# Optimization experiments

Hardware: AMD Instinct MI355X
Metric: run time of the kernel (lower is better)

Reference implementation:

```python
import jax, jax.numpy as jnp
import numpy as np

WEIGHT = 1.0  # configer affinity_loss weight


def setup_inputs() -> dict:
    key = jax.random.key(0)
    k1, k2, k3, k4, k5 = jax.random.split(key, 5)
    bz, C, h, w = 4, 21, 32, 32
    token_n = h * w            # 1024
    total_n = token_n + 1      # 1025 (CLS token in encoder attns)
    head_n = 8
    return {
        "preds": jax.random.normal(k1, (bz, C, h, w), dtype=jnp.float32),
        "low_feats": jnp.zeros((1,), dtype=jnp.float32),
        "high_feats": jnp.zeros((1,), dtype=jnp.float32),
        "unlabeled_ROIs": jax.random.randint(k2, (bz, h, w), 0, 2, dtype=jnp.int32),
        "targets": jax.random.randint(k3, (bz, h, w), 0, C),
        # raw (pre-renormalization) positive attention maps, stacked over 2 layers
        "attns": jax.random.uniform(k4, (2, bz, head_n, total_n, total_n), dtype=jnp.float32),
        "decode_attns": jax.random.uniform(k5, (2, bz, head_n, token_n, token_n), dtype=jnp.float32),
    }


def reference(preds, low_feats, high_feats, unlabeled_ROIs, targets, attns, decode_attns):
    # loss_index=2, gt_add=0
    bz, C, h, w = preds.shape
    token_n = h * w
    Le = attns.shape[0]
    Ld = decode_attns.shape[0]

    # Encoder attentions: drop CLS row/col, row-normalize, average over heads & layers.
    enc = attns[:, :, :, 1:, 1:]                         # (Le, b, H, t, t)
    enc = enc / enc.sum(axis=-1, keepdims=True)
    encode_attn_avg = enc.mean(axis=(0, 2))              # (b, t, t)

    # Decoder attentions: crop to token_n, row-normalize, average over heads & layers.
    dec = decode_attns[:, :, :, :token_n, :token_n]
    dec = dec / dec.sum(axis=-1, keepdims=True)
    decode_attn_avg = dec.mean(axis=(0, 2))              # (b, t, t)

    total_attn_avg = (encode_attn_avg * Le + decode_attn_avg * Ld) / (Le + Ld)

    # Class probabilities per token: (b, t, C)
    prob = jax.nn.softmax(preds, axis=1).reshape(bz, C, token_n).transpose(0, 2, 1)

    # The broadcast-multiply-sum over dim=2 is exactly a batched matmul.
    affinity_prob = jnp.einsum('bij,bjc->bic', total_attn_avg, prob)
    affinity_prob = affinity_prob / affinity_prob.sum(axis=-1, keepdims=True)

    # nearest-interp to (h, w) is the identity here (ROIs already at (h, w))
    roi = unlabeled_ROIs.astype(jnp.float32).reshape(bz, token_n, 1)
    N = roi.sum()
    loss = (roi * jnp.abs(prob - affinity_prob)).sum()
    loss = jnp.where(N > 0, loss / N, loss)
    return WEIGHT * loss
```

## Files before the change

### kernel.cpp

```cpp
#include <hip/hip_runtime.h>
#include <cstdint>
#include <cstddef>

#define C_N     21
#define BZ      4
#define TOKEN_N 1024
#define TOTAL_N 1025
#define PROB_ELEMS (BZ * TOKEN_N * C_N)
#define ENC_TOT  67240000u

typedef short  short8 __attribute__((ext_vector_type(8)));
typedef float  f32x4  __attribute__((ext_vector_type(4)));

static __device__ __forceinline__ unsigned int f2bf(float x) {
    unsigned int u = __float_as_uint(x);
    return (u + 0x7FFFu + ((u >> 16) & 1u)) >> 16;
}

__global__ __launch_bounds__(256) void softmax_kernel(const float* __restrict__ preds,
                                                      float* __restrict__ prob) {
    int t = blockIdx.x * blockDim.x + threadIdx.x;
    if (t >= BZ * TOKEN_N) return;
    int b = t >> 10, j = t & 1023;
    const float* p = preds + (size_t)b * C_N * TOKEN_N + j;
    float v[C_N];
    float mx = -3.4e38f;
#pragma unroll
    for (int c = 0; c < C_N; ++c) { v[c] = p[(size_t)c * TOKEN_N]; mx = fmaxf(mx, v[c]); }
    float ss = 0.f;
#pragma unroll
    for (int c = 0; c < C_N; ++c) { v[c] = __expf(v[c] - mx); ss += v[c]; }
    float inv = 1.f / ss;
    float* o = prob + (size_t)t * C_N;
#pragma unroll
    for (int c = 0; c < C_N; ++c) o[c] = v[c] * inv;
}

__global__ __launch_bounds__(256) void bpack2_kernel(const float* __restrict__ prob,
                                                     uint4* __restrict__ bp) {
    int idx = blockIdx.x * 256 + threadIdx.x;
    if (idx >= BZ * 32 * 2 * 64) return;
    int lane = idx & 63;
    int nt   = (idx >> 6) & 1;
    int kk   = (idx >> 7) & 31;
    int b    = idx >> 12;
    int n    = (lane & 15) + nt * 16;
    int k0   = kk * 32 + ((lane >> 4) << 3);
    unsigned int h[8];
#pragma unroll
    for (int e = 0; e < 8; ++e) {
        float v;
        if (n < C_N)       v = prob[((size_t)b * TOKEN_N + (k0 + e)) * C_N + n];
        else if (n == C_N) v = 1.0f;
        else               v = 0.0f;
        h[e] = f2bf(v);
    }
    uint4 o;
    o.x = h[0] | (h[1] << 16);
    o.y = h[2] | (h[3] << 16);
    o.z = h[4] | (h[5] << 16);
    o.w = h[6] | (h[7] << 16);
    bp[idx] = o;
}

template<bool ENC>
__device__ __forceinline__ void rows_body(const float* __restrict__ base, int mm, int lane,
                                          int i0, const uint4* __restrict__ bp,
                                          float* __restrict__ acc, float* __restrict__ ldsw) {
    constexpr int NSLOT = ENC ? 5 : 4;
    constexpr int D     = ENC ? 3 : 4;
    constexpr int RS    = 68;
    const int b = (mm >> 3) & 3;

    const float* gs[NSLOT];
    int lt[NSLOT];
#pragma unroll
    for (int s = 0; s < NSLOT; ++s) {
        if constexpr (ENC) {
            int t = (s == 4) ? (256 + (lane & 15)) : (s * 64 + lane);
            int row = t / 17, u = t - row * 17;
            size_t start = (size_t)mm * 1050625u + (size_t)(1 + i0 + row) * 1025u + 1u;
            int delta = (int)(start & 3);
            size_t gidx = start - delta + (size_t)u * 4;
            if (s == 4 && gidx > (size_t)(ENC_TOT - 964)) gidx = ENC_TOT - 964;
            gs[s] = base + gidx;
            lt[s] = t * 4;
        } else {
            int t = s * 64 + lane;
            int row = t >> 4, u = t & 15;
            gs[s] = base + (size_t)mm * 1048576u + (size_t)(i0 + row) * 1024u + (size_t)u * 4;
            lt[s] = row * RS + u * 4;
        }
    }

    float4 G[D][NSLOT];
    uint4  Bb[2][4];
    const uint4* bpp = bp + (size_t)b * 4096 + lane;

    const int r = lane & 15, kg = lane >> 4;
    int fragbase;
    if constexpr (ENC) fragbase = r * RS + ((mm + i0 + r + 2) & 3) + kg * 8;
    else               fragbase = r * RS + kg * 8;

    f32x4 c0 = {0.f, 0.f, 0.f, 0.f};
    f32x4 c1 = {0.f, 0.f, 0.f, 0.f};

    auto KSTEP = [&](const float* lf, int j0, uint4 bb0, uint4 bb1) {
        float a0, a1, a2, a3, a4, a5, a6, a7;
        if constexpr (ENC) {
            const float* p = lf + fragbase + j0;
            a0 = p[0]; a1 = p[1]; a2 = p[2]; a3 = p[3];
            a4 = p[4]; a5 = p[5]; a6 = p[6]; a7 = p[7];
        } else {
            float4 lo = *reinterpret_cast<const float4*>(lf + fragbase + j0);
            float4 hi = *reinterpret_cast<const float4*>(lf + fragbase + j0 + 4);
            a0 = lo.x; a1 = lo.y; a2 = lo.z; a3 = lo.w;
            a4 = hi.x; a5 = hi.y; a6 = hi.z; a7 = hi.w;
        }
        uint4 aw;
        aw.x = f2bf(a0) | (f2bf(a1) << 16);
        aw.y = f2bf(a2) | (f2bf(a3) << 16);
        aw.z = f2bf(a4) | (f2bf(a5) << 16);
        aw.w = f2bf(a6) | (f2bf(a7) << 16);
        short8 af = __builtin_bit_cast(short8, aw);
        c0 = __builtin_amdgcn_mfma_f32_16x16x32_bf16(af, __builtin_bit_cast(short8, bb0), c0, 0, 0, 0);
        c1 = __builtin_amdgcn_mfma_f32_16x16x32_bf16(af, __builtin_bit_cast(short8, bb1), c1, 0, 0, 0);
    };

#pragma unroll
    for (int s = 0; s < D; ++s)
#pragma unroll
        for (int q = 0; q < NSLOT; ++q)
            G[s][q] = *reinterpret_cast<const float4*>(gs[q] + s * 64);
#pragma unroll
    for (int q = 0; q < 4; ++q) Bb[0][q] = bpp[q * 64];
    {
        float* d0 = ldsw;
#pragma unroll
        for (int q = 0; q < NSLOT; ++q)
            *reinterpret_cast<float4*>(d0 + lt[q]) = G[0][q];
    }
#pragma unroll
    for (int q = 0; q < 4; ++q) Bb[1][q] = bpp[256 + q * 64];

#pragma unroll
    for (int k = 0; k < 16; ++k) {
        const float* lf = ldsw + (k & 1) * 1088;
        KSTEP(lf, 0,  Bb[k & 1][0], Bb[k & 1][1]);
        KSTEP(lf, 32, Bb[k & 1][2], Bb[k & 1][3]);
        if (k < 15) {
            float* d = ldsw + ((k + 1) & 1) * 1088;
#pragma unroll
            for (int q = 0; q < NSLOT; ++q)
                *reinterpret_cast<float4*>(d + lt[q]) = G[(k + 1) % D][q];
        }
        if (k + D < 16) {
#pragma unroll
            for (int q = 0; q < NSLOT; ++q)
                G[k % D][q] = *reinterpret_cast<const float4*>(gs[q] + (k + D) * 64);
        }
        if (k + 2 < 16) {
#pragma unroll
            for (int q = 0; q < 4; ++q) Bb[k & 1][q] = bpp[(k + 2) * 256 + q * 64];
        }
    }

#pragma unroll
    for (int rr = 0; rr < 4; ++rr) {
        float sv  = __shfl(c1[rr], (lane & 48) + 5);
        float inv = 1.0f / sv;
        int i = i0 + kg * 4 + rr;
        float* ao = acc + ((size_t)b * TOKEN_N + i) * C_N;
        unsafeAtomicAdd(&ao[r], c0[rr] * inv);
        if (r < C_N - 16) unsafeAtomicAdd(&ao[16 + r], c1[rr] * inv);
    }
}

__global__ __launch_bounds__(256) void rows6_kernel(const float* __restrict__ attns,
                                                    const float* __restrict__ dattns,
                                                    const uint4* __restrict__ bp,
                                                    float* __restrict__ acc) {
    __shared__ __align__(16) float lds[8704];
    const int lane = threadIdx.x & 63;
    const int wv   = threadIdx.x >> 6;
    float* ldsw = lds + wv * 2176;
    const int wid  = blockIdx.x * 4 + wv;
    const int m    = wid >> 6;
    const int i0   = (wid & 63) << 4;
    if (m < 64) rows_body<true >(attns,  m,      lane, i0, bp, acc, ldsw);
    else        rows_body<false>(dattns, m - 64, lane, i0, bp, acc, ldsw);
}

__global__ __launch_bounds__(256) void loss_kernel(const float* __restrict__ prob,
                                                   const float* __restrict__ acc,
                                                   const int* __restrict__ roi,
                                                   float* __restrict__ scal) {
    int t = blockIdx.x * 256 + threadIdx.x;
    float lossp = 0.f, np = 0.f;
    if (t < BZ * TOKEN_N) {
        int rv = roi[t];
        np = (float)rv;
        const float* a = acc + (size_t)t * C_N;
        const float* p = prob + (size_t)t * C_N;
        float S = 0.f;
#pragma unroll
        for (int c = 0; c < C_N; ++c) S += a[c];
        float invS = 1.f / S;
        float l = 0.f;
#pragma unroll
        for (int c = 0; c < C_N; ++c) l += fabsf(p[c] - a[c] * invS);
        lossp = rv ? l : 0.f;
    }
#pragma unroll
    for (int off = 32; off > 0; off >>= 1) {
        lossp += __shfl_down(lossp, off);
        np    += __shfl_down(np, off);
    }
    __shared__ float redL[4], redN[4];
    int lane = threadIdx.x & 63, wv = threadIdx.x >> 6;
    if (lane == 0) { redL[wv] = lossp; redN[wv] = np; }
    __syncthreads();
    if (threadIdx.x == 0) {
        float L  = redL[0] + redL[1] + redL[2] + redL[3];
        float NN = redN[0] + redN[1] + redN[2] + redN[3];
        unsafeAtomicAdd(&scal[0], L);
        unsafeAtomicAdd(&scal[1], NN);
    }
}

__global__ void finalize_kernel(const float* __restrict__ scal, float* __restrict__ out) {
    float loss = scal[0], N = scal[1];
    out[0] = (N > 0.f) ? (loss / N) : loss;
}

extern "C" void kernel_launch(void* const* d_in, const int* in_sizes, int n_in,
                              void* d_out, int out_size, void* d_ws, size_t ws_size,
                              hipStream_t stream) {
    const float* preds  = (const float*)d_in[0];
    const int*   roi    = (const int*)d_in[3];
    const float* attns  = (const float*)d_in[5];
    const float* dattns = (const float*)d_in[6];

    float* prob = (float*)d_ws;
    float* acc  = prob + PROB_ELEMS;
    float* scal = acc + PROB_ELEMS;
    uint4* bpack = (uint4*)((char*)d_ws + ((PROB_ELEMS * 2 + 2) * sizeof(float) + 15 & ~(size_t)15));

    hipMemsetAsync(acc, 0, (PROB_ELEMS + 2) * sizeof(float), stream);

    hipLaunchKernelGGL(softmax_kernel, dim3((BZ * TOKEN_N + 255) / 256), dim3(256), 0, stream,
                       preds, prob);
    hipLaunchKernelGGL(bpack2_kernel, dim3(64), dim3(256), 0, stream,
                       prob, bpack);
    hipLaunchKernelGGL(rows6_kernel, dim3(2048), dim3(256), 0, stream,
                       attns, dattns, bpack, acc);
    hipLaunchKernelGGL(loss_kernel, dim3((BZ * TOKEN_N + 255) / 256), dim3(256), 0, stream,
                       prob, acc, roi, scal);
    hipLaunchKernelGGL(finalize_kernel, dim3(1), dim3(1), 0, stream,
                       scal, (float*)d_out);
}
```

Measured before the change: 129.7 us.

## Load attention row tiles directly into LDS and split K across waves

```diff
diff --git a/kernel.cpp b/kernel.cpp
--- a/kernel.cpp
+++ b/kernel.cpp
@@ -7,10 +7,13 @@
 #define TOKEN_N 1024
 #define TOTAL_N 1025
 #define PROB_ELEMS (BZ * TOKEN_N * C_N)
-#define ENC_TOT  67240000u
+#define ENC_TOT  67240000ull
 
 typedef short  short8 __attribute__((ext_vector_type(8)));
 typedef float  f32x4  __attribute__((ext_vector_type(4)));
+
+typedef __attribute__((address_space(1))) const unsigned int* gld_gp;
+typedef __attribute__((address_space(3))) unsigned int*       gld_lp;
 
 static __device__ __forceinline__ unsigned int f2bf(float x) {
     unsigned int u = __float_as_uint(x);
@@ -64,56 +67,70 @@
 }
 
 template<bool ENC>
-__device__ __forceinline__ void rows_body(const float* __restrict__ base, int mm, int lane,
-                                          int i0, const uint4* __restrict__ bp,
-                                          float* __restrict__ acc, float* __restrict__ ldsw) {
-    constexpr int NSLOT = ENC ? 5 : 4;
-    constexpr int D     = ENC ? 3 : 4;
-    constexpr int RS    = 68;
-    const int b = (mm >> 3) & 3;
-
-    const float* gs[NSLOT];
-    int lt[NSLOT];
-#pragma unroll
-    for (int s = 0; s < NSLOT; ++s) {
-        if constexpr (ENC) {
-            int t = (s == 4) ? (256 + (lane & 15)) : (s * 64 + lane);
-            int row = t / 17, u = t - row * 17;
-            size_t start = (size_t)mm * 1050625u + (size_t)(1 + i0 + row) * 1025u + 1u;
-            int delta = (int)(start & 3);
-            size_t gidx = start - delta + (size_t)u * 4;
-            if (s == 4 && gidx > (size_t)(ENC_TOT - 964)) gidx = ENC_TOT - 964;
-            gs[s] = base + gidx;
-            lt[s] = t * 4;
-        } else {
-            int t = s * 64 + lane;
-            int row = t >> 4, u = t & 15;
-            gs[s] = base + (size_t)mm * 1048576u + (size_t)(i0 + row) * 1024u + (size_t)u * 4;
-            lt[s] = row * RS + u * 4;
-        }
-    }
-
-    float4 G[D][NSLOT];
-    uint4  Bb[2][4];
+__device__ __forceinline__ void rows_body(const float* __restrict__ base, int mm, int i0,
+                                          const uint4* __restrict__ bp,
+                                          float* __restrict__ acc, float* __restrict__ lds) {
+    const int tid  = threadIdx.x;
+    const int lane = tid & 63;
+    const int w    = tid >> 6;
+    const int b    = (mm >> 3) & 3;
+
+    int delta = 0;
+    if constexpr (ENC) {
+        const size_t S0 = (size_t)mm * 1050625ull + (size_t)(1 + i0) * 1025ull + 1ull;
+        const size_t aligned = S0 & ~(size_t)3;
+        delta = (int)(S0 - aligned);
+        const int nInstr = (w < 3) ? 17 : 14;
+        const int e0 = w * 17;
+        for (int q = 0; q < nInstr; ++q) {
+            const int e = e0 + q;
+            size_t gb  = aligned + (size_t)e * 256;
+            int   ldso = e * 256;
+            if (gb + 256 > ENC_TOT) {
+                size_t d = gb + 256 - ENC_TOT;
+                gb -= d; ldso -= (int)d;
+            }
+            __builtin_amdgcn_global_load_lds((gld_gp)(base + gb + (size_t)lane * 4),
+                                             (gld_lp)&lds[ldso], 16, 0, 0);
+        }
+    } else {
+        const size_t sb = (size_t)mm * 1048576ull + (size_t)i0 * 1024ull;
+#pragma unroll
+        for (int q = 0; q < 16; ++q) {
+            const int e = w * 16 + q;
+            const int row = e >> 2, sub = e & 3;
+            const size_t gb = sb + (size_t)row * 1024 + (size_t)sub * 256;
+            const int ldso  = row * 1028 + sub * 256;
+            __builtin_amdgcn_global_load_lds((gld_gp)(base + gb + (size_t)lane * 4),
+                                             (gld_lp)&lds[ldso], 16, 0, 0);
+        }
+    }
+
     const uint4* bpp = bp + (size_t)b * 4096 + lane;
+    uint4 Bq[8][2];
+#pragma unroll
+    for (int s = 0; s < 8; ++s) {
+        Bq[s][0] = bpp[(w * 8 + s) * 128];
+        Bq[s][1] = bpp[(w * 8 + s) * 128 + 64];
+    }
+
+    __syncthreads();
 
     const int r = lane & 15, kg = lane >> 4;
-    int fragbase;
-    if constexpr (ENC) fragbase = r * RS + ((mm + i0 + r + 2) & 3) + kg * 8;
-    else               fragbase = r * RS + kg * 8;
-
     f32x4 c0 = {0.f, 0.f, 0.f, 0.f};
     f32x4 c1 = {0.f, 0.f, 0.f, 0.f};
-
-    auto KSTEP = [&](const float* lf, int j0, uint4 bb0, uint4 bb1) {
+#pragma unroll
+    for (int s = 0; s < 8; ++s) {
+        const int k0 = w * 256 + s * 32 + kg * 8;
         float a0, a1, a2, a3, a4, a5, a6, a7;
         if constexpr (ENC) {
-            const float* p = lf + fragbase + j0;
+            const float* p = lds + delta + r * 1025 + k0;
             a0 = p[0]; a1 = p[1]; a2 = p[2]; a3 = p[3];
             a4 = p[4]; a5 = p[5]; a6 = p[6]; a7 = p[7];
         } else {
-            float4 lo = *reinterpret_cast<const float4*>(lf + fragbase + j0);
-            float4 hi = *reinterpret_cast<const float4*>(lf + fragbase + j0 + 4);
+            const float* p = lds + r * 1028 + k0;
+            float4 lo = *reinterpret_cast<const float4*>(p);
+            float4 hi = *reinterpret_cast<const float4*>(p + 4);
             a0 = lo.x; a1 = lo.y; a2 = lo.z; a3 = lo.w;
             a4 = hi.x; a5 = hi.y; a6 = hi.z; a7 = hi.w;
         }
@@ -123,72 +140,46 @@
         aw.z = f2bf(a4) | (f2bf(a5) << 16);
         aw.w = f2bf(a6) | (f2bf(a7) << 16);
         short8 af = __builtin_bit_cast(short8, aw);
-        c0 = __builtin_amdgcn_mfma_f32_16x16x32_bf16(af, __builtin_bit_cast(short8, bb0), c0, 0, 0, 0);
-        c1 = __builtin_amdgcn_mfma_f32_16x16x32_bf16(af, __builtin_bit_cast(short8, bb1), c1, 0, 0, 0);
-    };
-
-#pragma unroll
-    for (int s = 0; s < D; ++s)
-#pragma unroll
-        for (int q = 0; q < NSLOT; ++q)
-            G[s][q] = *reinterpret_cast<const float4*>(gs[q] + s * 64);
-#pragma unroll
-    for (int q = 0; q < 4; ++q) Bb[0][q] = bpp[q * 64];
-    {
-        float* d0 = ldsw;
-#pragma unroll
-        for (int q = 0; q < NSLOT; ++q)
-            *reinterpret_cast<float4*>(d0 + lt[q]) = G[0][q];
-    }
-#pragma unroll
-    for (int q = 0; q < 4; ++q) Bb[1][q] = bpp[256 + q * 64];
-
-#pragma unroll
-    for (int k = 0; k < 16; ++k) {
-        const float* lf = ldsw + (k & 1) * 1088;
-        KSTEP(lf, 0,  Bb[k & 1][0], Bb[k & 1][1]);
-        KSTEP(lf, 32, Bb[k & 1][2], Bb[k & 1][3]);
-        if (k < 15) {
-            float* d = ldsw + ((k + 1) & 1) * 1088;
-#pragma unroll
-            for (int q = 0; q < NSLOT; ++q)
-                *reinterpret_cast<float4*>(d + lt[q]) = G[(k + 1) % D][q];
-        }
-        if (k + D < 16) {
-#pragma unroll
-            for (int q = 0; q < NSLOT; ++q)
-                G[k % D][q] = *reinterpret_cast<const float4*>(gs[q] + (k + D) * 64);
-        }
-        if (k + 2 < 16) {
-#pragma unroll
-            for (int q = 0; q < 4; ++q) Bb[k & 1][q] = bpp[(k + 2) * 256 + q * 64];
-        }
-    }
-
-#pragma unroll
-    for (int rr = 0; rr < 4; ++rr) {
-        float sv  = __shfl(c1[rr], (lane & 48) + 5);
-        float inv = 1.0f / sv;
-        int i = i0 + kg * 4 + rr;
-        float* ao = acc + ((size_t)b * TOKEN_N + i) * C_N;
-        unsafeAtomicAdd(&ao[r], c0[rr] * inv);
-        if (r < C_N - 16) unsafeAtomicAdd(&ao[16 + r], c1[rr] * inv);
-    }
-}
-
-__global__ __launch_bounds__(256) void rows6_kernel(const float* __restrict__ attns,
+        c0 = __builtin_amdgcn_mfma_f32_16x16x32_bf16(af, __builtin_bit_cast(short8, Bq[s][0]), c0, 0, 0, 0);
+        c1 = __builtin_amdgcn_mfma_f32_16x16x32_bf16(af, __builtin_bit_cast(short8, Bq[s][1]), c1, 0, 0, 0);
+    }
+
+    __syncthreads();
+    if (w != 0) {
+        float* red = lds + w * 512 + lane * 8;
+#pragma unroll
+        for (int j = 0; j < 4; ++j) { red[j] = c0[j]; red[4 + j] = c1[j]; }
+    }
+    __syncthreads();
+    if (w == 0) {
+#pragma unroll
+        for (int ww = 1; ww < 4; ++ww) {
+            const float* red = lds + ww * 512 + lane * 8;
+#pragma unroll
+            for (int j = 0; j < 4; ++j) { c0[j] += red[j]; c1[j] += red[4 + j]; }
+        }
+#pragma unroll
+        for (int rr = 0; rr < 4; ++rr) {
+            float sv  = __shfl(c1[rr], (lane & 48) + 5);
+            float inv = 1.0f / sv;
+            int i = i0 + kg * 4 + rr;
+            float* ao = acc + ((size_t)b * TOKEN_N + i) * C_N;
+            unsafeAtomicAdd(&ao[r], c0[rr] * inv);
+            if (r < C_N - 16) unsafeAtomicAdd(&ao[16 + r], c1[rr] * inv);
+        }
+    }
+}
+
+__global__ __launch_bounds__(256) void rows7_kernel(const float* __restrict__ attns,
                                                     const float* __restrict__ dattns,
                                                     const uint4* __restrict__ bp,
                                                     float* __restrict__ acc) {
-    __shared__ __align__(16) float lds[8704];
-    const int lane = threadIdx.x & 63;
-    const int wv   = threadIdx.x >> 6;
-    float* ldsw = lds + wv * 2176;
-    const int wid  = blockIdx.x * 4 + wv;
-    const int m    = wid >> 6;
-    const int i0   = (wid & 63) << 4;
-    if (m < 64) rows_body<true >(attns,  m,      lane, i0, bp, acc, ldsw);
-    else        rows_body<false>(dattns, m - 64, lane, i0, bp, acc, ldsw);
+    __shared__ __align__(16) float lds[16640];
+    const int wid = blockIdx.x;
+    const int m   = wid >> 6;
+    const int i0  = (wid & 63) << 4;
+    if (m < 64) rows_body<true >(attns,  m,      i0, bp, acc, lds);
+    else        rows_body<false>(dattns, m - 64, i0, bp, acc, lds);
 }
 
 __global__ __launch_bounds__(256) void loss_kernel(const float* __restrict__ prob,
@@ -252,7 +243,7 @@
                        preds, prob);
     hipLaunchKernelGGL(bpack2_kernel, dim3(64), dim3(256), 0, stream,
                        prob, bpack);
-    hipLaunchKernelGGL(rows6_kernel, dim3(2048), dim3(256), 0, stream,
+    hipLaunchKernelGGL(rows7_kernel, dim3(8192), dim3(256), 0, stream,
                        attns, dattns, bpack, acc);
     hipLaunchKernelGGL(loss_kernel, dim3((BZ * TOKEN_N + 255) / 256), dim3(256), 0, stream,
                        prob, acc, roi, scal);
```

Result: no change. 127.4 us (-1.8%).
